# Optimization experiments

Measured on AMD Instinct MI355X. Metric: run time of the kernel, lower is better.

The kernel has to match this reference:

```python
import jax, jax.numpy as jnp
import numpy as np

DIM = 1024

def setup_inputs() -> dict:
    key = jax.random.key(0)
    k1, k2, k3, k4 = jax.random.split(key, 4)
    B, L, D = 32, 2048, DIM
    x = jax.random.normal(k1, (B, D), dtype=jnp.float32)
    context = jax.random.normal(k2, (B, L, D), dtype=jnp.float32)
    # linear_concatWa: Linear(2*dim, dim, bias=False) -> weight [dim, 2*dim]
    Wa = jax.random.normal(k3, (D, 2 * D), dtype=jnp.float32) * (1.0 / np.sqrt(2 * D))
    # linear_concatVa: Linear(dim, 1, bias=False) -> weight [1, dim]
    Va = jax.random.normal(k4, (1, D), dtype=jnp.float32) * (1.0 / np.sqrt(D))
    return {"x": x, "context": context, "Wa": Wa, "Va": Va}


def reference(x, context, Wa, Va):
    # concat-mode additive (Bahdanau) attention.
    # Wa @ cat(ht, hs) == ht @ Wa[:, :D].T + hs @ Wa[:, D:].T  (avoids materializing concat)
    D = x.shape[-1]
    Wa_t, Wa_s = Wa[:, :D], Wa[:, D:]              # each [D, D]
    ht_proj = jnp.einsum('bd,kd->bk', x, Wa_t)     # [B, D]
    hs_proj = jnp.einsum('bld,kd->blk', context, Wa_s)  # [B, L, D]
    hidden = jnp.tanh(ht_proj[:, None, :] + hs_proj)    # [B, L, D]
    scores = jnp.einsum('blk,ok->bl', hidden, Va)       # [B, L]  (Va: [1, D])
    attn = jax.nn.softmax(scores, axis=-1)               # [B, L]
    weighted = jnp.einsum('bl,bld->bd', attn, context)   # [B, D]
    return weighted, attn
```

## Files before the change

### kernel.cpp

```cpp
#include <hip/hip_runtime.h>
#include <hip/hip_bf16.h>
#include <cstdint>
#include <cstddef>

#define DIM 1024
#define B_SZ 32
#define L_SZ 2048

#define BM 128
#define BN 128

#define CVT_BLOCKS 8192
#define HT_BLOCKS  512
#define WA_BLOCKS  512

typedef __attribute__((ext_vector_type(8))) short bf16x8;
typedef __attribute__((ext_vector_type(4))) float floatx4;

static __device__ __forceinline__ unsigned cvt2_bf16_rne(float a, float b) {
    unsigned ua = __builtin_bit_cast(unsigned, a);
    unsigned ub = __builtin_bit_cast(unsigned, b);
    ua = (ua + 0x7FFFu + ((ua >> 16) & 1u)) >> 16;
    ub = (ub + 0x7FFFu + ((ub >> 16) & 1u)) >> 16;
    return ua | (ub << 16);
}

static __device__ __forceinline__ float bf2f(unsigned u16) {
    return __builtin_bit_cast(float, u16 << 16);
}

static __device__ __forceinline__ float tanh_fast(float x) {
    float e = __expf(2.0f * x);
    return 1.0f - 2.0f * __builtin_amdgcn_rcpf(e + 1.0f);
}

static __device__ __forceinline__ void gld_lds16(const void* g, void* lds) {
    __builtin_amdgcn_global_load_lds(
        (const __attribute__((address_space(1))) unsigned int*)g,
        (__attribute__((address_space(3))) unsigned int*)lds,
        16, 0, 0);
}

#define VMCNT(n) asm volatile("s_waitcnt vmcnt(" #n ")" ::: "memory")
#define BARRIER() __builtin_amdgcn_s_barrier()

__global__ __launch_bounds__(256) void pre_kernel(
    const float* __restrict__ x, const float* __restrict__ ctx,
    const float* __restrict__ Wa,
    unsigned short* __restrict__ ctxB, unsigned short* __restrict__ WaB,
    float* __restrict__ ht, float* __restrict__ scores,
    float* __restrict__ weighted)
{
    const int bid = blockIdx.x, t = threadIdx.x;

    if (bid < CVT_BLOCKS) {
        const long n8 = (long)B_SZ * L_SZ * DIM / 8;
        const long stride = (long)CVT_BLOCKS * 256;
        for (long i = (long)bid * 256 + t; i < n8; i += stride) {
            const float4 a = ((const float4*)ctx)[i * 2];
            const float4 b = ((const float4*)ctx)[i * 2 + 1];
            uint4 o;
            o.x = cvt2_bf16_rne(a.x, a.y);
            o.y = cvt2_bf16_rne(a.z, a.w);
            o.z = cvt2_bf16_rne(b.x, b.y);
            o.w = cvt2_bf16_rne(b.z, b.w);
            ((uint4*)ctxB)[i] = o;
        }
    } else if (bid < CVT_BLOCKS + HT_BLOCKS) {
        const int lb = bid - CVT_BLOCKS;
        const int gi = lb * 256 + t;
        if (gi < B_SZ * L_SZ) scores[gi] = 0.f;
        const int b = lb >> 4, kb = lb & 15;
        __shared__ float xs[DIM];
        for (int i = t; i < DIM; i += 256) xs[i] = x[b * DIM + i];
        __syncthreads();
        const int wave = t >> 6, lane = t & 63;
        const float4* xs4 = (const float4*)xs;
        for (int kk = 0; kk < 16; ++kk) {
            const int k = kb * 64 + wave * 16 + kk;
            const float4* wr = (const float4*)(Wa + (size_t)k * (2 * DIM));
            float s = 0.f;
            #pragma unroll
            for (int d = 0; d < DIM / 4; d += 64) {
                const float4 w4 = wr[d + lane];
                const float4 x4 = xs4[d + lane];
                s += w4.x * x4.x + w4.y * x4.y + w4.z * x4.z + w4.w * x4.w;
            }
            #pragma unroll
            for (int off = 32; off > 0; off >>= 1) s += __shfl_xor(s, off);
            if (lane == 0) ht[b * DIM + k] = s;
        }
    } else {
        const int lb = bid - CVT_BLOCKS - HT_BLOCKS;
        const int i = lb * 256 + t;
        if (i < B_SZ * DIM) weighted[i] = 0.f;
        const int k = i >> 7, dc = i & 127;
        const float* s = Wa + (size_t)k * (2 * DIM) + DIM + dc * 8;
        const float4 a = ((const float4*)s)[0];
        const float4 b4 = ((const float4*)s)[1];
        uint4 o;
        o.x = cvt2_bf16_rne(a.x, a.y);
        o.y = cvt2_bf16_rne(a.z, a.w);
        o.z = cvt2_bf16_rne(b4.x, b4.y);
        o.w = cvt2_bf16_rne(b4.z, b4.w);
        ((uint4*)(WaB + (size_t)k * DIM + dc * 8))[0] = o;
    }
}

static __device__ __forceinline__ void frag_loads_a(
    const unsigned short* sh, int wr, int l15, int quad, bf16x8 (&af)[4][2])
{
    #pragma unroll
    for (int i = 0; i < 4; ++i) {
        const int r = wr + i * 16 + l15;
        #pragma unroll
        for (int kb = 0; kb < 2; ++kb) {
            const int c = (kb * 4 + quad) ^ (r & 7);
            af[i][kb] = *(const bf16x8*)&sh[r * 64 + c * 8];
        }
    }
}

static __device__ __forceinline__ void frag_loads_b(
    const unsigned short* sh, int wc, int l15, int quad, bf16x8 (&bv)[2][2])
{
    #pragma unroll
    for (int j = 0; j < 2; ++j) {
        const int r = wc + j * 16 + l15;
        #pragma unroll
        for (int kb = 0; kb < 2; ++kb) {
            const int c = (kb * 4 + quad) ^ (r & 7);
            bv[j][kb] = *(const bf16x8*)&sh[r * 64 + c * 8];
        }
    }
}

static __device__ __forceinline__ void mma16(
    floatx4 (&acc)[4][2], const bf16x8 (&af)[4][2], const bf16x8 (&bv)[2][2])
{
    __builtin_amdgcn_s_setprio(1);
    #pragma unroll
    for (int kb = 0; kb < 2; ++kb)
        #pragma unroll
        for (int i = 0; i < 4; ++i)
            #pragma unroll
            for (int j = 0; j < 2; ++j)
                acc[i][j] = __builtin_amdgcn_mfma_f32_16x16x32_bf16(
                    af[i][kb], bv[j][kb], acc[i][j], 0, 0, 0);
    __builtin_amdgcn_s_setprio(0);
}

static __device__ __forceinline__ void stage_half(
    const unsigned short* __restrict__ g, unsigned short* lds, int t, int wave)
{
    #pragma unroll
    for (int q = 0; q < 2; ++q) {
        const int ch = q * 512 + t;
        const int lr = ch >> 3;
        const int lc = (ch & 7) ^ (lr & 7);
        gld_lds16(g + (size_t)lr * DIM + lc * 8, lds + (q * 512 + wave * 64) * 8);
    }
}

__global__ __launch_bounds__(512, 2) void gemm_score_8ph(
    const unsigned short* __restrict__ A, const unsigned short* __restrict__ Bm,
    const float* __restrict__ Va, const float* __restrict__ ht,
    float* __restrict__ scores)
{
    __shared__ __align__(16) unsigned short As[2][2][128 * 64];
    __shared__ __align__(16) unsigned short Bs[2][2][128 * 64];

    const int bid = blockIdx.x;
    const int logical = (bid & 7) * 128 + (bid >> 3);
    const int m0 = (logical >> 2) * 256;
    const int n0 = (logical & 3) * 256;

    const int t = threadIdx.x;
    const int lane = t & 63, wave = t >> 6;
    const int l15 = lane & 15, quad = lane >> 4;
    const int wr = (wave >> 2) * 64;
    const int wc = (wave & 3) * 32;

    const unsigned short* Ag = A + (size_t)m0 * DIM;
    const unsigned short* Bg = Bm + (size_t)n0 * DIM;

    floatx4 acc[4][4][2];
    #pragma unroll
    for (int q = 0; q < 4; ++q)
        #pragma unroll
        for (int i = 0; i < 4; ++i)
            #pragma unroll
            for (int j = 0; j < 2; ++j) acc[q][i][j] = (floatx4)0.f;

    bf16x8 af[4][2], bv[2][2];

    stage_half(Ag, &As[0][0][0], t, wave);
    stage_half(Bg, &Bs[0][0][0], t, wave);
    stage_half(Bg + (size_t)128 * DIM, &Bs[0][1][0], t, wave);
    stage_half(Ag + (size_t)128 * DIM, &As[0][1][0], t, wave);
    stage_half(Ag + 64, &As[1][0][0], t, wave);
    stage_half(Bg + (size_t)128 * DIM + 64, &Bs[1][1][0], t, wave);
    VMCNT(4);
    BARRIER();

    for (int it = 0; it < 8; ++it) {
        const int k1 = (2 * it + 1) * 64;
        const int k2 = (2 * it + 2) * 64;
        const int k3 = (2 * it + 3) * 64;
        const bool more = (it < 7);

        frag_loads_a(&As[0][0][0], wr, l15, quad, af);
        frag_loads_b(&Bs[0][0][0], wc, l15, quad, bv);
        stage_half(Bg + k1, &Bs[1][0][0], t, wave);
        stage_half(Ag + (size_t)128 * DIM + k1, &As[1][1][0], t, wave);
        BARRIER();
        mma16(acc[0], af, bv);
        BARRIER();

        frag_loads_b(&Bs[0][1][0], wc, l15, quad, bv);
        BARRIER();
        mma16(acc[1], af, bv);
        BARRIER();

        frag_loads_a(&As[0][1][0], wr, l15, quad, af);
        BARRIER();
        mma16(acc[3], af, bv);
        BARRIER();

        frag_loads_b(&Bs[0][0][0], wc, l15, quad, bv);
        if (more) { stage_half(Ag + k2, &As[0][0][0], t, wave); VMCNT(2); }
        else      { VMCNT(0); }
        BARRIER();
        mma16(acc[2], af, bv);
        BARRIER();

        frag_loads_a(&As[1][0][0], wr, l15, quad, af);
        frag_loads_b(&Bs[1][0][0], wc, l15, quad, bv);
        if (more) stage_half(Bg + (size_t)128 * DIM + k2, &Bs[0][1][0], t, wave);
        BARRIER();
        mma16(acc[0], af, bv);
        BARRIER();

        frag_loads_b(&Bs[1][1][0], wc, l15, quad, bv);
        if (more) stage_half(Ag + (size_t)128 * DIM + k2, &As[0][1][0], t, wave);
        BARRIER();
        mma16(acc[1], af, bv);
        BARRIER();

        frag_loads_a(&As[1][1][0], wr, l15, quad, af);
        if (more) {
            stage_half(Bg + k2, &Bs[0][0][0], t, wave);
            stage_half(Ag + k3, &As[1][0][0], t, wave);
        }
        BARRIER();
        mma16(acc[3], af, bv);
        BARRIER();

        frag_loads_b(&Bs[1][0][0], wc, l15, quad, bv);
        if (more) {
            stage_half(Bg + (size_t)128 * DIM + k3, &Bs[1][1][0], t, wave);
            VMCNT(4);
        }
        BARRIER();
        mma16(acc[2], af, bv);
        BARRIER();
    }

    const int bb = m0 >> 11;
    float htv[2][2], vav[2][2];
    #pragma unroll
    for (int qc = 0; qc < 2; ++qc)
        #pragma unroll
        for (int j = 0; j < 2; ++j) {
            const int ng = n0 + qc * 128 + wc + j * 16 + l15;
            htv[qc][j] = ht[bb * DIM + ng];
            vav[qc][j] = Va[ng];
        }
    #pragma unroll
    for (int qr = 0; qr < 2; ++qr)
        #pragma unroll
        for (int i = 0; i < 4; ++i)
            #pragma unroll
            for (int r = 0; r < 4; ++r) {
                float s = 0.f;
                #pragma unroll
                for (int qc = 0; qc < 2; ++qc)
                    #pragma unroll
                    for (int j = 0; j < 2; ++j)
                        s += tanh_fast(acc[qr * 2 + qc][i][j][r] + htv[qc][j]) * vav[qc][j];
                s += __shfl_xor(s, 8);
                s += __shfl_xor(s, 4);
                s += __shfl_xor(s, 2);
                s += __shfl_xor(s, 1);
                if (l15 == 0)
                    atomicAdd(&scores[m0 + qr * 128 + wr + i * 16 + quad * 4 + r], s);
            }
}

__global__ __launch_bounds__(256) void post_kernel(
    const float* __restrict__ scores, const unsigned short* __restrict__ ctxB,
    float* __restrict__ attn, float* __restrict__ weighted)
{
    const int b = blockIdx.x, slice = blockIdx.y, t = threadIdx.x;
    const float* sc = scores + b * L_SZ;
    __shared__ float red[256];
    __shared__ float att[128];

    float m = -1e30f;
    for (int l = t; l < L_SZ; l += 256) m = fmaxf(m, sc[l]);
    red[t] = m; __syncthreads();
    for (int s = 128; s > 0; s >>= 1) { if (t < s) red[t] = fmaxf(red[t], red[t + s]); __syncthreads(); }
    m = red[0]; __syncthreads();
    float sum = 0.f;
    for (int l = t; l < L_SZ; l += 256) sum += __expf(sc[l] - m);
    red[t] = sum; __syncthreads();
    for (int s = 128; s > 0; s >>= 1) { if (t < s) red[t] += red[t + s]; __syncthreads(); }
    const float inv = 1.0f / red[0];

    const int l0 = slice * 128;
    if (t < 128) {
        const float av = __expf(sc[l0 + t] - m) * inv;
        att[t] = av;
        attn[b * L_SZ + l0 + t] = av;
    }
    __syncthreads();

    const unsigned short* cb = ctxB + ((size_t)b * L_SZ + l0) * DIM + t * 4;
    float a0 = 0.f, a1 = 0.f, a2 = 0.f, a3 = 0.f;
    for (int l = 0; l < 128; ++l) {
        const float a = att[l];
        const uint2 v = *(const uint2*)(cb + (size_t)l * DIM);
        a0 += a * bf2f(v.x & 0xFFFFu);
        a1 += a * bf2f(v.x >> 16);
        a2 += a * bf2f(v.y & 0xFFFFu);
        a3 += a * bf2f(v.y >> 16);
    }
    float* o = weighted + b * DIM + t * 4;
    atomicAdd(o + 0, a0);
    atomicAdd(o + 1, a1);
    atomicAdd(o + 2, a2);
    atomicAdd(o + 3, a3);
}

#define LDS_STRIDE 40
__global__ __launch_bounds__(256) void ht_kernel_fb(const float* __restrict__ x,
                                                    const float* __restrict__ Wa,
                                                    float* __restrict__ ht,
                                                    float* __restrict__ scores,
                                                    float* __restrict__ weighted) {
    const int b = blockIdx.x, kb = blockIdx.y, t = threadIdx.x;
    const int gidx = (b * 16 + kb) * 256 + t;
    if (gidx < B_SZ * L_SZ) scores[gidx] = 0.f;
    if (gidx < B_SZ * DIM) weighted[gidx] = 0.f;
    __shared__ float xs[DIM];
    for (int i = t; i < DIM; i += 256) xs[i] = x[b * DIM + i];
    __syncthreads();
    const int wave = t >> 6, lane = t & 63;
    for (int kk = 0; kk < 16; ++kk) {
        const int k = kb * 64 + wave * 16 + kk;
        const float* wr = Wa + (size_t)k * (2 * DIM);
        float s = 0.f;
        #pragma unroll
        for (int d = 0; d < DIM; d += 64) s += xs[d + lane] * wr[d + lane];
        #pragma unroll
        for (int off = 32; off > 0; off >>= 1) s += __shfl_xor(s, off);
        if (lane == 0) ht[b * DIM + k] = s;
    }
}

__global__ __launch_bounds__(256, 2) void gemm_score_kernel(
    const float* __restrict__ ctx, const float* __restrict__ Wa,
    const float* __restrict__ Va, const float* __restrict__ ht,
    float* __restrict__ scores)
{
    __shared__ unsigned short As[BM * LDS_STRIDE];
    __shared__ unsigned short Bs[BN * LDS_STRIDE];
    const int t = threadIdx.x;
    const int n0 = blockIdx.x * BN;
    const int m0 = blockIdx.y * BM;
    const int lane = t & 63, wave = t >> 6;
    const int l15 = lane & 15, quad = lane >> 4;
    const int wm = (wave >> 1) * 64, wn = (wave & 1) * 64;
    const int srow = t >> 3;
    const int scol = (t & 7) * 4;
    const float* aBase = ctx + (size_t)(m0 + srow) * DIM + scol;
    const float* bBase = Wa + (size_t)(n0 + srow) * (2 * DIM) + DIM + scol;

    floatx4 acc[4][4];
    #pragma unroll
    for (int i = 0; i < 4; ++i)
        #pragma unroll
        for (int j = 0; j < 4; ++j) acc[i][j] = (floatx4)0.f;

    for (int k0 = 0; k0 < DIM; k0 += 32) {
        __syncthreads();
        #pragma unroll
        for (int r = 0; r < 4; ++r) {
            const float4 va = *(const float4*)(aBase + (size_t)(r * 32) * DIM + k0);
            const float4 vb = *(const float4*)(bBase + (size_t)(r * 32) * (2 * DIM) + k0);
            *(uint2*)&As[(srow + r * 32) * LDS_STRIDE + scol] =
                make_uint2(cvt2_bf16_rne(va.x, va.y), cvt2_bf16_rne(va.z, va.w));
            *(uint2*)&Bs[(srow + r * 32) * LDS_STRIDE + scol] =
                make_uint2(cvt2_bf16_rne(vb.x, vb.y), cvt2_bf16_rne(vb.z, vb.w));
        }
        __syncthreads();
        bf16x8 af[4], bfr[4];
        #pragma unroll
        for (int i = 0; i < 4; ++i)
            af[i] = *(const bf16x8*)&As[(wm + i * 16 + l15) * LDS_STRIDE + quad * 8];
        #pragma unroll
        for (int j = 0; j < 4; ++j)
            bfr[j] = *(const bf16x8*)&Bs[(wn + j * 16 + l15) * LDS_STRIDE + quad * 8];
        #pragma unroll
        for (int i = 0; i < 4; ++i)
            #pragma unroll
            for (int j = 0; j < 4; ++j)
                acc[i][j] = __builtin_amdgcn_mfma_f32_16x16x32_bf16(af[i], bfr[j], acc[i][j], 0, 0, 0);
    }
    const int bb = m0 >> 11;
    float htv[4], vav[4];
    #pragma unroll
    for (int j = 0; j < 4; ++j) {
        const int ng = n0 + wn + j * 16 + l15;
        htv[j] = ht[bb * DIM + ng];
        vav[j] = Va[ng];
    }
    #pragma unroll
    for (int i = 0; i < 4; ++i) {
        #pragma unroll
        for (int r = 0; r < 4; ++r) {
            float s = 0.f;
            #pragma unroll
            for (int j = 0; j < 4; ++j)
                s += tanh_fast(acc[i][j][r] + htv[j]) * vav[j];
            s += __shfl_xor(s, 8);
            s += __shfl_xor(s, 4);
            s += __shfl_xor(s, 2);
            s += __shfl_xor(s, 1);
            if (l15 == 0)
                atomicAdd(&scores[m0 + wm + i * 16 + quad * 4 + r], s);
        }
    }
}

__global__ __launch_bounds__(256) void post_kernel_fb(
    const float* __restrict__ scores, const float* __restrict__ ctx,
    float* __restrict__ attn, float* __restrict__ weighted)
{
    const int b = blockIdx.x, slice = blockIdx.y, t = threadIdx.x;
    const float* sc = scores + b * L_SZ;
    __shared__ float red[256];
    __shared__ float att[128];
    float m = -1e30f;
    for (int l = t; l < L_SZ; l += 256) m = fmaxf(m, sc[l]);
    red[t] = m; __syncthreads();
    for (int s = 128; s > 0; s >>= 1) { if (t < s) red[t] = fmaxf(red[t], red[t + s]); __syncthreads(); }
    m = red[0]; __syncthreads();
    float sum = 0.f;
    for (int l = t; l < L_SZ; l += 256) sum += __expf(sc[l] - m);
    red[t] = sum; __syncthreads();
    for (int s = 128; s > 0; s >>= 1) { if (t < s) red[t] += red[t + s]; __syncthreads(); }
    const float inv = 1.0f / red[0];
    const int l0 = slice * 128;
    if (t < 128) {
        const float av = __expf(sc[l0 + t] - m) * inv;
        att[t] = av;
        attn[b * L_SZ + l0 + t] = av;
    }
    __syncthreads();
    const float* cb = ctx + ((size_t)b * L_SZ + l0) * DIM + t * 4;
    float4 w = make_float4(0.f, 0.f, 0.f, 0.f);
    for (int l = 0; l < 128; ++l) {
        const float a = att[l];
        const float4 c = *(const float4*)(cb + (size_t)l * DIM);
        w.x += a * c.x; w.y += a * c.y; w.z += a * c.z; w.w += a * c.w;
    }
    float* o = weighted + b * DIM + t * 4;
    atomicAdd(o + 0, w.x);
    atomicAdd(o + 1, w.y);
    atomicAdd(o + 2, w.z);
    atomicAdd(o + 3, w.w);
}

extern "C" void kernel_launch(void* const* d_in, const int* in_sizes, int n_in,
                              void* d_out, int out_size, void* d_ws, size_t ws_size,
                              hipStream_t stream) {
    const float* x   = (const float*)d_in[0];
    const float* ctx = (const float*)d_in[1];
    const float* Wa  = (const float*)d_in[2];
    const float* Va  = (const float*)d_in[3];

    float* out      = (float*)d_out;
    float* weighted = out;
    float* attn     = out + B_SZ * DIM;

    float* scores = (float*)d_ws;
    float* ht     = scores + B_SZ * L_SZ;

    const size_t base = (size_t)(B_SZ * L_SZ + B_SZ * DIM) * sizeof(float);
    const size_t need = base + (size_t)DIM * DIM * 2
                      + (size_t)B_SZ * L_SZ * DIM * 2;

    if (ws_size >= need) {
        unsigned short* WaB  = (unsigned short*)((char*)d_ws + base);
        unsigned short* ctxB = WaB + (size_t)DIM * DIM;
        pre_kernel<<<CVT_BLOCKS + HT_BLOCKS + WA_BLOCKS, 256, 0, stream>>>(
            x, ctx, Wa, ctxB, WaB, ht, scores, weighted);
        gemm_score_8ph<<<(B_SZ * L_SZ / 256) * (DIM / 256), 512, 0, stream>>>(
            ctxB, WaB, Va, ht, scores);
        post_kernel<<<dim3(B_SZ, 16), 256, 0, stream>>>(scores, ctxB, attn, weighted);
    } else {
        ht_kernel_fb<<<dim3(B_SZ, 16), 256, 0, stream>>>(x, Wa, ht, scores, weighted);
        gemm_score_kernel<<<dim3(DIM / BN, (B_SZ * L_SZ) / BM), 256, 0, stream>>>(
            ctx, Wa, Va, ht, scores);
        post_kernel_fb<<<dim3(B_SZ, 16), 256, 0, stream>>>(scores, ctx, attn, weighted);
    }
}
```

Measured before the change: 586.8 us.

## Cache B fragments in two register sets and use inline-asm LDS reads

Replaces compiler-generated LDS fragment loads with inline ds_read_b128 on precomputed LDS byte addresses, followed by explicit lgkmcnt waits and sched barriers. B fragments are kept in two register sets (bvA/bvB), which removes two of the eight per-half-iteration B reloads. The global staging of Bs[0][0] is moved earlier in the schedule. This cuts LDS traffic and gives tighter control over instruction ordering, at the cost of more VGPRs and correctness that now depends on hand-placed waits around the moved stage writes.

```diff
diff --git a/kernel.cpp b/kernel.cpp
--- a/kernel.cpp
+++ b/kernel.cpp
@@ -41,8 +41,16 @@
         16, 0, 0);
 }
 
-#define VMCNT(n) asm volatile("s_waitcnt vmcnt(" #n ")" ::: "memory")
-#define BARRIER() __builtin_amdgcn_s_barrier()
+static __device__ __forceinline__ bf16x8 dsr128(unsigned addr) {
+    bf16x8 r;
+    asm volatile("ds_read_b128 %0, %1" : "=v"(r) : "v"(addr));
+    return r;
+}
+
+#define VMCNT(n)  asm volatile("s_waitcnt vmcnt(" #n ")" ::: "memory")
+#define SBAR()    asm volatile("s_barrier" ::: "memory")
+#define WAITK()   do { asm volatile("s_waitcnt lgkmcnt(0)" ::: "memory"); \
+                       __builtin_amdgcn_sched_barrier(0); } while (0)
 
 __global__ __launch_bounds__(256) void pre_kernel(
     const float* __restrict__ x, const float* __restrict__ ctx,
@@ -107,8 +115,8 @@
     }
 }
 
-static __device__ __forceinline__ void frag_loads_a(
-    const unsigned short* sh, int wr, int l15, int quad, bf16x8 (&af)[4][2])
+static __device__ __forceinline__ void lda4(
+    unsigned base, int wr, int l15, int quad, bf16x8 (&af)[4][2])
 {
     #pragma unroll
     for (int i = 0; i < 4; ++i) {
@@ -116,13 +124,13 @@
         #pragma unroll
         for (int kb = 0; kb < 2; ++kb) {
             const int c = (kb * 4 + quad) ^ (r & 7);
-            af[i][kb] = *(const bf16x8*)&sh[r * 64 + c * 8];
-        }
-    }
-}
-
-static __device__ __forceinline__ void frag_loads_b(
-    const unsigned short* sh, int wc, int l15, int quad, bf16x8 (&bv)[2][2])
+            af[i][kb] = dsr128(base + (unsigned)(r * 128 + c * 16));
+        }
+    }
+}
+
+static __device__ __forceinline__ void ldb2(
+    unsigned base, int wc, int l15, int quad, bf16x8 (&bv)[2][2])
 {
     #pragma unroll
     for (int j = 0; j < 2; ++j) {
@@ -130,7 +138,7 @@
         #pragma unroll
         for (int kb = 0; kb < 2; ++kb) {
             const int c = (kb * 4 + quad) ^ (r & 7);
-            bv[j][kb] = *(const bf16x8*)&sh[r * 64 + c * 8];
+            bv[j][kb] = dsr128(base + (unsigned)(r * 128 + c * 16));
         }
     }
 }
@@ -184,6 +192,11 @@
     const unsigned short* Ag = A + (size_t)m0 * DIM;
     const unsigned short* Bg = Bm + (size_t)n0 * DIM;
 
+    const unsigned aB = (unsigned)(unsigned long long)&As[0][0][0];
+    const unsigned bB = (unsigned)(unsigned long long)&Bs[0][0][0];
+    const unsigned a00 = aB, a01 = aB + 16384, a10 = aB + 32768, a11 = aB + 49152;
+    const unsigned b00 = bB, b01 = bB + 16384, b10 = bB + 32768, b11 = bB + 49152;
+
     floatx4 acc[4][4][2];
     #pragma unroll
     for (int q = 0; q < 4; ++q)
@@ -192,7 +205,7 @@
             #pragma unroll
             for (int j = 0; j < 2; ++j) acc[q][i][j] = (floatx4)0.f;
 
-    bf16x8 af[4][2], bv[2][2];
+    bf16x8 af[4][2], bvA[2][2], bvB[2][2];
 
     stage_half(Ag, &As[0][0][0], t, wave);
     stage_half(Bg, &Bs[0][0][0], t, wave);
@@ -201,7 +214,7 @@
     stage_half(Ag + 64, &As[1][0][0], t, wave);
     stage_half(Bg + (size_t)128 * DIM + 64, &Bs[1][1][0], t, wave);
     VMCNT(4);
-    BARRIER();
+    SBAR();
 
     for (int it = 0; it < 8; ++it) {
         const int k1 = (2 * it + 1) * 64;
@@ -209,61 +222,63 @@
         const int k3 = (2 * it + 3) * 64;
         const bool more = (it < 7);
 
-        frag_loads_a(&As[0][0][0], wr, l15, quad, af);
-        frag_loads_b(&Bs[0][0][0], wc, l15, quad, bv);
+        lda4(a00, wr, l15, quad, af);
+        ldb2(b00, wc, l15, quad, bvA);
         stage_half(Bg + k1, &Bs[1][0][0], t, wave);
+        SBAR();
+        WAITK();
+        mma16(acc[0], af, bvA);
+        SBAR();
+
+        ldb2(b01, wc, l15, quad, bvB);
         stage_half(Ag + (size_t)128 * DIM + k1, &As[1][1][0], t, wave);
-        BARRIER();
-        mma16(acc[0], af, bv);
-        BARRIER();
-
-        frag_loads_b(&Bs[0][1][0], wc, l15, quad, bv);
-        BARRIER();
-        mma16(acc[1], af, bv);
-        BARRIER();
-
-        frag_loads_a(&As[0][1][0], wr, l15, quad, af);
-        BARRIER();
-        mma16(acc[3], af, bv);
-        BARRIER();
-
-        frag_loads_b(&Bs[0][0][0], wc, l15, quad, bv);
+        if (more) stage_half(Bg + k2, &Bs[0][0][0], t, wave);
+        SBAR();
+        WAITK();
+        mma16(acc[1], af, bvB);
+        SBAR();
+
+        lda4(a01, wr, l15, quad, af);
+        SBAR();
+        WAITK();
+        mma16(acc[3], af, bvB);
+        SBAR();
+
         if (more) { stage_half(Ag + k2, &As[0][0][0], t, wave); VMCNT(2); }
         else      { VMCNT(0); }
-        BARRIER();
-        mma16(acc[2], af, bv);
-        BARRIER();
-
-        frag_loads_a(&As[1][0][0], wr, l15, quad, af);
-        frag_loads_b(&Bs[1][0][0], wc, l15, quad, bv);
+        SBAR();
+        mma16(acc[2], af, bvA);
+        SBAR();
+
+        lda4(a10, wr, l15, quad, af);
+        ldb2(b10, wc, l15, quad, bvA);
         if (more) stage_half(Bg + (size_t)128 * DIM + k2, &Bs[0][1][0], t, wave);
-        BARRIER();
-        mma16(acc[0], af, bv);
-        BARRIER();
-
-        frag_loads_b(&Bs[1][1][0], wc, l15, quad, bv);
+        SBAR();
+        WAITK();
+        mma16(acc[0], af, bvA);
+        SBAR();
+
+        ldb2(b11, wc, l15, quad, bvB);
         if (more) stage_half(Ag + (size_t)128 * DIM + k2, &As[0][1][0], t, wave);
-        BARRIER();
-        mma16(acc[1], af, bv);
-        BARRIER();
-
-        frag_loads_a(&As[1][1][0], wr, l15, quad, af);
-        if (more) {
-            stage_half(Bg + k2, &Bs[0][0][0], t, wave);
-            stage_half(Ag + k3, &As[1][0][0], t, wave);
-        }
-        BARRIER();
-        mma16(acc[3], af, bv);
-        BARRIER();
-
-        frag_loads_b(&Bs[1][0][0], wc, l15, quad, bv);
+        SBAR();
+        WAITK();
+        mma16(acc[1], af, bvB);
+        SBAR();
+
+        lda4(a11, wr, l15, quad, af);
+        if (more) stage_half(Ag + k3, &As[1][0][0], t, wave);
+        SBAR();
+        WAITK();
+        mma16(acc[3], af, bvB);
+        SBAR();
+
         if (more) {
             stage_half(Bg + (size_t)128 * DIM + k3, &Bs[1][1][0], t, wave);
             VMCNT(4);
         }
-        BARRIER();
-        mma16(acc[2], af, bv);
-        BARRIER();
+        SBAR();
+        mma16(acc[2], af, bvA);
+        SBAR();
     }
 
     const int bb = m0 >> 11;
```

Result: slower. 617.1 us (+5.2%).
